# Optimization experiments

Hardware: AMD Instinct MI355X
Metric: run time of the kernel (lower is better)

The kernel has to match this reference:

```python
import jax, jax.numpy as jnp
import numpy as np

EMBED_DIM = 512
NUM_HEADS = 8
GLOBAL_MIX = 0.5


def setup_inputs() -> dict:
    key = jax.random.key(0)
    ks = jax.random.split(key, 7)
    B, L, E = 8, 1024, EMBED_DIM
    s = 1.0 / np.sqrt(E)
    x = jax.random.normal(ks[0], (B, L, E), dtype=jnp.float32)
    mask = jax.random.randint(ks[1], (B, L), 0, 2) > 0  # True = valid token
    Wq = jax.random.normal(ks[2], (E, E), dtype=jnp.float32) * s
    Wk = jax.random.normal(ks[3], (E, E), dtype=jnp.float32) * s
    Wv = jax.random.normal(ks[4], (E, E), dtype=jnp.float32) * s
    Wo = jax.random.normal(ks[5], (E, E), dtype=jnp.float32) * s
    G = jax.random.normal(ks[6], (L, L), dtype=jnp.float32)
    return {"x": x, "mask": mask, "Wq": Wq, "Wk": Wk, "Wv": Wv, "Wo": Wo, "G": G}


def _tanh_mha(x, mask, Wq, Wk, Wv, Wo, G):
    B, L, E = x.shape
    H = NUM_HEADS
    D = E // H
    scale = 1.0 / np.sqrt(D)
    dt = x.dtype
    fmax = jnp.finfo(dt).max
    tiny = jnp.finfo(dt).tiny

    def split_heads(t):  # (B,L,E) -> (B,H,L,D)
        return t.reshape(B, L, H, D).transpose(0, 2, 1, 3)

    q = split_heads(x @ Wq.T)
    k = split_heads(x @ Wk.T)
    v = split_heads(x @ Wv.T)

    scores = jnp.tanh(jnp.einsum('bhqd,bhkd->bhqk', q, k) * scale)
    key_valid = mask[:, None, None, :]  # (B,1,1,L)
    scores = jnp.where(key_valid, scores, -jnp.inf)

    finite = jnp.isfinite(scores)
    finite_scores = jnp.where(finite, scores, -fmax)
    m = jnp.max(finite_scores, axis=(1, 2, 3), keepdims=True)  # per-sample amax over heads+q+k
    m = jnp.where(jnp.isfinite(m), m, jnp.zeros_like(m))
    exp_scores = jnp.where(finite, jnp.exp(scores - m), jnp.zeros_like(scores))

    mf = mask.astype(dt)
    exp_scores = exp_scores * mf[:, None, None, :] * mf[:, None, :, None]
    denom = jnp.maximum(exp_scores.sum(axis=(1, 2, 3), keepdims=True), tiny)
    weights = exp_scores / denom
    # dropout p=0 -> identity; renorm pass kept for faithfulness
    renorm = jnp.maximum(weights.sum(axis=(1, 2, 3), keepdims=True), tiny)
    weights = weights / renorm

    # learnable global attention: softmax rows, clamp, mask, normalize over (q,k)
    activated = jnp.maximum(jax.nn.softmax(G, axis=-1), 0.0)  # (L,L)
    gscores = activated[None] * mf[:, None, :] * mf[:, :, None]  # (B,L,L)
    gsums = jnp.maximum(gscores.sum(axis=(1, 2), keepdims=True), tiny)
    gnorm = (gscores / gsums)[:, None]  # (B,1,L,L)
    weights = (1.0 - GLOBAL_MIX) * weights + GLOBAL_MIX * gnorm

    attended = jnp.einsum('bhqk,bhkd->bhqd', weights, v)
    attended = attended * mf[:, None, :, None]
    attended = attended.transpose(0, 2, 1, 3).reshape(B, L, E)
    return attended @ Wo.T


def reference(x, mask, Wq, Wk, Wv, Wo, G):
    return _tanh_mha(x, mask, Wq, Wk, Wv, Wo, G)
```

## Files before the change

kernel.cpp:

```cpp
#include <hip/hip_runtime.h>
#include <math.h>

#define B_ 8
#define L_ 1024
#define E_ 512
#define H_ 8
#define D_ 64
#define QSZ (B_*H_*L_*D_)
#define TINYF 1.175494350822287508e-38f

typedef unsigned short u16;
typedef __attribute__((ext_vector_type(8))) short bfrag;
typedef __attribute__((ext_vector_type(4))) float ffrag;
typedef __attribute__((ext_vector_type(16))) float ffrag16;
typedef __attribute__((ext_vector_type(4))) short vshort4;

#if __has_builtin(__builtin_amdgcn_exp2f)
#define EXP2F(x) __builtin_amdgcn_exp2f(x)
#else
#define EXP2F(x) __expf((x) * 0.6931471805599453f)
#endif
#if __has_builtin(__builtin_amdgcn_rcpf)
#define RCPF(x) __builtin_amdgcn_rcpf(x)
#else
#define RCPF(x) (1.0f / (x))
#endif

__device__ __forceinline__ u16 f2b(float f) {
  unsigned u = __float_as_uint(f);
  u += 0x7fffu + ((u >> 16) & 1u);
  return (u16)(u >> 16);
}
__device__ __forceinline__ unsigned pk2(float a, float b) {
  unsigned ua = __float_as_uint(a); ua += 0x7fffu + ((ua >> 16) & 1u);
  unsigned ub = __float_as_uint(b); ub += 0x7fffu + ((ub >> 16) & 1u);
  return (ua >> 16) | (ub & 0xffff0000u);
}
__device__ __forceinline__ float b2f(unsigned h) { return __uint_as_float(h << 16); }
__device__ __forceinline__ float blo(unsigned u) { return __uint_as_float(u << 16); }
__device__ __forceinline__ float bhi(unsigned u) { return __uint_as_float(u & 0xffff0000u); }

__device__ __forceinline__ bfrag cvt8v(const float* __restrict__ src) {
  float4 a = *(const float4*)src;
  float4 b = *(const float4*)(src + 4);
  bfrag r;
  r[0]=(short)f2b(a.x); r[1]=(short)f2b(a.y); r[2]=(short)f2b(a.z); r[3]=(short)f2b(a.w);
  r[4]=(short)f2b(b.x); r[5]=(short)f2b(b.y); r[6]=(short)f2b(b.z); r[7]=(short)f2b(b.w);
  return r;
}

__device__ __forceinline__ void gll16(const void* g, void* l) {
  __builtin_amdgcn_global_load_lds(
      (const __attribute__((address_space(1))) void*)g,
      (__attribute__((address_space(3))) void*)l, 16, 0, 0);
}

__global__ __launch_bounds__(256) void prep_k(
    const float* __restrict__ x, const float* __restrict__ Wq,
    const float* __restrict__ Wk, const float* __restrict__ Wv,
    const float* __restrict__ Wo, u16* __restrict__ xb, u16* __restrict__ Wb,
    float* __restrict__ sums) {
  const int bid = blockIdx.x, t = threadIdx.x;
  if (bid == 0 && t < 16) sums[t] = 0.0f;
  if (bid < 2048) {
    size_t c = (size_t)bid * 256 + t;
    *(bfrag*)&xb[c * 8] = cvt8v(x + c * 8);
  } else {
    const int c2 = bid - 2048;
    const float* src = (c2 < 128) ? Wq : (c2 < 256) ? Wk : (c2 < 384) ? Wv : Wo;
    const size_t base = (size_t)(c2 >> 7) * 262144;
    const size_t cc = (size_t)(c2 & 127) * 256 + t;
    *(bfrag*)&Wb[base + cc * 8] = cvt8v(src + cc * 8);
  }
}

__global__ __launch_bounds__(256) void softmax_g_k(
    const float* __restrict__ G, const int* __restrict__ mask,
    u16* __restrict__ actb, float* __restrict__ R) {
  const int q = blockIdx.x, t = threadIdx.x;
  const int w = t >> 6, lane = t & 63;
  __shared__ float sred[8];
  __shared__ float rred[4][8];
  float4 g4 = ((const float4*)(G + (size_t)q * 1024))[t];
  float m = fmaxf(fmaxf(g4.x, g4.y), fmaxf(g4.z, g4.w));
#pragma unroll
  for (int off = 32; off > 0; off >>= 1) m = fmaxf(m, __shfl_down(m, off));
  if (lane == 0) sred[w] = m;
  __syncthreads();
  m = fmaxf(fmaxf(sred[0], sred[1]), fmaxf(sred[2], sred[3]));
  float e0 = __expf(g4.x - m), e1 = __expf(g4.y - m);
  float e2 = __expf(g4.z - m), e3 = __expf(g4.w - m);
  float s = e0 + e1 + e2 + e3;
#pragma unroll
  for (int off = 32; off > 0; off >>= 1) s += __shfl_down(s, off);
  if (lane == 0) sred[4 + w] = s;
  __syncthreads();
  const float inv = 1.0f / (sred[4] + sred[5] + sred[6] + sred[7]);
  const unsigned p0 = pk2(e0 * inv, e1 * inv);
  const unsigned p1 = pk2(e2 * inv, e3 * inv);
  *(uint2*)&actb[(size_t)q * 1024 + t * 4] = make_uint2(p0, p1);
  const float r0 = blo(p0), r1 = bhi(p0);
  const float r2 = blo(p1), r3 = bhi(p1);
  float rd[8];
#pragma unroll
  for (int b = 0; b < 8; ++b) {
    const int* mkp = mask + b * 1024 + t * 4;
    rd[b] = (mkp[0] ? r0 : 0.f) + (mkp[1] ? r1 : 0.f) +
            (mkp[2] ? r2 : 0.f) + (mkp[3] ? r3 : 0.f);
#pragma unroll
    for (int off = 32; off > 0; off >>= 1) rd[b] += __shfl_down(rd[b], off);
  }
  if (lane == 0)
#pragma unroll
    for (int b = 0; b < 8; ++b) rred[w][b] = rd[b];
  __syncthreads();
  if (t < 8) R[q * 8 + t] = rred[0][t] + rred[1][t] + rred[2][t] + rred[3][t];
}

__global__ __launch_bounds__(256) void gsum_reduce_k(
    const float* __restrict__ R, const int* __restrict__ mask,
    float* __restrict__ sums) {
  const int t = threadIdx.x, w = t >> 6, lane = t & 63;
  __shared__ float rr[4][8];
  float acc[8] = {0,0,0,0,0,0,0,0};
  for (int q = t; q < 1024; q += 256)
#pragma unroll
    for (int b = 0; b < 8; ++b)
      if (mask[b * 1024 + q]) acc[b] += R[q * 8 + b];
#pragma unroll
  for (int b = 0; b < 8; ++b) {
#pragma unroll
    for (int off = 32; off > 0; off >>= 1) acc[b] += __shfl_down(acc[b], off);
  }
  if (lane == 0)
#pragma unroll
    for (int b = 0; b < 8; ++b) rr[w][b] = acc[b];
  __syncthreads();
  if (t < 8) sums[8 + t] = rr[0][t] + rr[1][t] + rr[2][t] + rr[3][t];
}

__global__ __launch_bounds__(256) void proj_k(
    const u16* __restrict__ xb, const u16* __restrict__ Wb,
    const int* __restrict__ mask,
    u16* __restrict__ Qb, u16* __restrict__ Kb, u16* __restrict__ Vtb) {
  const int m0 = blockIdx.x * 128;
  const int n0 = blockIdx.y * 64;
  __shared__ u16 As[128 * 64];
  __shared__ u16 Bs[64 * 64];
  const int t = threadIdx.x, w = t >> 6, lane = t & 63;
  const int l15 = lane & 15, quad = lane >> 4;
  const int x7 = l15 & 7;
  const ffrag fz = {0.f, 0.f, 0.f, 0.f};
  ffrag acc[2][4];
#pragma unroll
  for (int am = 0; am < 2; ++am)
#pragma unroll
    for (int bn = 0; bn < 4; ++bn) acc[am][bn] = fz;

  for (int kk = 0; kk < 512; kk += 64) {
    __syncthreads();
#pragma unroll
    for (int j = 0; j < 4; ++j) {
      const int c = w * 256 + j * 64 + lane;
      const int row = c >> 3, ck = (c & 7) ^ (row & 7);
      gll16(xb + (size_t)(m0 + row) * 512 + kk + ck * 8,
            &As[(size_t)(w * 256 + j * 64) * 8]);
    }
#pragma unroll
    for (int j = 0; j < 2; ++j) {
      const int c = w * 128 + j * 64 + lane;
      const int row = c >> 3, ck = (c & 7) ^ (row & 7);
      gll16(Wb + (size_t)(n0 + row) * 512 + kk + ck * 8,
            &Bs[(size_t)(w * 128 + j * 64) * 8]);
    }
    __syncthreads();
#pragma unroll
    for (int s = 0; s < 2; ++s) {
      const int co = ((quad + 4 * s) ^ x7) << 3;
      bfrag a0 = *(const bfrag*)&As[(w * 32 + l15) * 64 + co];
      bfrag a1 = *(const bfrag*)&As[(w * 32 + 16 + l15) * 64 + co];
#pragma unroll
      for (int bn = 0; bn < 4; ++bn) {
        bfrag bb = *(const bfrag*)&Bs[(bn * 16 + l15) * 64 + co];
        acc[0][bn] = __builtin_amdgcn_mfma_f32_16x16x32_bf16(a0, bb, acc[0][bn], 0, 0, 0);
        acc[1][bn] = __builtin_amdgcn_mfma_f32_16x16x32_bf16(a1, bb, acc[1][bn], 0, 0, 0);
      }
    }
  }
  const int z = n0 >> 9;
  const int c0 = n0 & 511;
#pragma unroll
  for (int am = 0; am < 2; ++am) {
    const int mbase = m0 + w * 32 + am * 16 + quad * 4;
    const int b = mbase >> 10, l0 = mbase & 1023;
#pragma unroll
    for (int bn = 0; bn < 4; ++bn) {
      const int nc = c0 + bn * 16 + l15;
      const int h = nc >> 6, d = nc & 63;
      if (z == 0) {
        u16* dst = Qb + ((size_t)(b * 8 + h) * 1024 + l0) * 64 + d;
#pragma unroll
        for (int r = 0; r < 4; ++r) dst[(size_t)r * 64] = f2b(acc[am][bn][r]);
      } else if (z == 1) {
        u16* dst = Kb + ((size_t)(b * 8 + h) * 1024 + l0) * 64 + d;
#pragma unroll
        for (int r = 0; r < 4; ++r) dst[(size_t)r * 64] = f2b(acc[am][bn][r]);
      } else {
        vshort4 vs;
#pragma unroll
        for (int r = 0; r < 4; ++r)
          vs[r] = (short)(mask[b * 1024 + l0 + r] ? f2b(acc[am][bn][r]) : (u16)0);
        *(vshort4*)(Vtb + ((size_t)(b * 8 + h) * 64 + d) * 1024 + l0) = vs;
      }
    }
  }
}

__global__ __launch_bounds__(256) void attn_k(
    const u16* __restrict__ Qb, const u16* __restrict__ Kb,
    const u16* __restrict__ Vtb, const u16* __restrict__ actb,
    const int* __restrict__ mask,
    u16* __restrict__ AEb, u16* __restrict__ AGb, float* __restrict__ denom) {
  const int qt = blockIdx.x;
  const int bh = blockIdx.y;
  const int b = bh >> 3, h = bh & 7;
  __shared__ __align__(16) u16 Ks[64 * 64];
  __shared__ __align__(16) u16 Vs[64 * 64];
  __shared__ __align__(16) u16 Acts[64 * 64];
  __shared__ __align__(16) u16 Es[64 * 64];
  __shared__ __align__(16) u16 Ms[16 * 64];
  const int t = threadIdx.x, w = t >> 6, lane = t & 63;
  const int l31 = lane & 31, hi = lane >> 5;
  const int qsb = w >> 1, msb = w & 1;
  const int qpb = w & 1, dpb = w >> 1;

  const u16* Kg = Kb + (size_t)bh * 65536;
  const u16* Vg = Vtb + (size_t)bh * 65536;
  const u16* Ag = actb + (size_t)(qt * 64) * 1024;

  const u16* Qrow = Qb + ((size_t)bh * 1024 + qt * 64 + qsb * 32 + l31) * 64;
  bfrag qf[4];
#pragma unroll
  for (int ko = 0; ko < 4; ++ko) qf[ko] = *(const bfrag*)(Qrow + ko * 16 + hi * 8);

  {
    int4 mi = *(const int4*)(mask + b * 1024 + t * 4);
    vshort4 mv;
    mv[0] = mi.x ? (short)0x3F80 : (short)0; mv[1] = mi.y ? (short)0x3F80 : (short)0;
    mv[2] = mi.z ? (short)0x3F80 : (short)0; mv[3] = mi.w ? (short)0x3F80 : (short)0;
    *(vshort4*)&Ms[t * 4] = mv;
  }

  auto stageK = [&](int kt) {
#pragma unroll
    for (int j = 0; j < 2; ++j) {
      const int c = w * 128 + j * 64 + lane;
      const int row = c >> 3, ck = (c & 7) ^ (row & 7);
      gll16(Kg + (size_t)(kt * 64 + row) * 64 + ck * 8,
            &Ks[(size_t)(w * 128 + j * 64) * 8]);
    }
  };
  auto stageV = [&](int kt) {
#pragma unroll
    for (int j = 0; j < 2; ++j) {
      const int c = w * 128 + j * 64 + lane;
      const int row = c >> 3, ck = (c & 7) ^ (row & 7);
      gll16(Vg + (size_t)row * 1024 + kt * 64 + ck * 8,
            &Vs[(size_t)(w * 128 + j * 64) * 8]);
    }
  };
  auto stageA = [&](int kt) {
#pragma unroll
    for (int j = 0; j < 2; ++j) {
      const int c = w * 128 + j * 64 + lane;
      const int row = c >> 3, ck = (c & 7) ^ (row & 7);
      gll16(Ag + (size_t)row * 1024 + kt * 64 + ck * 8,
            &Acts[(size_t)(w * 128 + j * 64) * 8]);
    }
  };

  stageK(0); stageV(0); stageA(0);
  __syncthreads();

  ffrag16 accE = {0.f}, accG = {0.f}, dacc = {0.f};
#pragma unroll
  for (int i = 0; i < 16; ++i) { accE[i] = 0.f; accG[i] = 0.f; dacc[i] = 0.f; }

  for (int kt = 0; kt < 16; ++kt) {
    ffrag16 st;
#pragma unroll
    for (int i = 0; i < 16; ++i) st[i] = 0.f;
    const int krow = msb * 32 + l31;
    const int kx7 = krow & 7;
#pragma unroll
    for (int ko = 0; ko < 4; ++ko) {
      bfrag ak = *(const bfrag*)&Ks[krow * 64 + (((ko * 2 + hi) ^ kx7) << 3)];
      st = __builtin_amdgcn_mfma_f32_32x32x16_bf16(ak, qf[ko], st, 0, 0, 0);
    }
    const int qrow = qsb * 32 + l31;
    const int qx7 = qrow & 7;
#pragma unroll
    for (int g = 0; g < 4; ++g) {
      float ee[4];
#pragma unroll
      for (int r = 0; r < 4; ++r) {
        const float tt = EXP2F(st[4 * g + r] * 0.360673760222f);
        ee[r] = EXP2F(RCPF(tt + 1.0f) * -2.88539008178f);
      }
      const int k0 = msb * 32 + g * 8 + hi * 4;
      *(uint2*)&Es[qrow * 64 + (((k0 >> 3) ^ qx7) << 3) + (k0 & 7)] =
          make_uint2(pk2(ee[0], ee[1]), pk2(ee[2], ee[3]));
    }
    __syncthreads();
    if (kt < 15) stageK(kt + 1);

    const int erow = qpb * 32 + l31;
    const int ex7 = erow & 7;
    const int vrow = dpb * 32 + l31;
    const int vx7 = vrow & 7;
#pragma unroll
    for (int ko = 0; ko < 4; ++ko) {
      const int ecs = ((ko * 2 + hi) ^ ex7) << 3;
      const int vcs = ((ko * 2 + hi) ^ vx7) << 3;
      bfrag ea = *(const bfrag*)&Es[erow * 64 + ecs];
      bfrag bv = *(const bfrag*)&Vs[vrow * 64 + vcs];
      accE = __builtin_amdgcn_mfma_f32_32x32x16_bf16(ea, bv, accE, 0, 0, 0);
      bfrag aa = *(const bfrag*)&Acts[erow * 64 + ecs];
      accG = __builtin_amdgcn_mfma_f32_32x32x16_bf16(aa, bv, accG, 0, 0, 0);
      if (w < 2) {
        bfrag bm = *(const bfrag*)&Ms[kt * 64 + ko * 16 + hi * 8];
        dacc = __builtin_amdgcn_mfma_f32_32x32x16_bf16(ea, bm, dacc, 0, 0, 0);
      }
    }
    __syncthreads();
    if (kt < 15) { stageV(kt + 1); stageA(kt + 1); }
  }

  const size_t obase = ((size_t)b * 1024 + qt * 64 + qpb * 32) * 512
                       + h * 64 + dpb * 32 + l31;
#pragma unroll
  for (int r = 0; r < 16; ++r) {
    const int qloc = (r & 3) + 8 * (r >> 2) + 4 * hi;
    AEb[obase + (size_t)qloc * 512] = f2b(accE[r]);
    AGb[obase + (size_t)qloc * 512] = f2b(accG[r]);
  }
  float dsumv = 0.0f;
  if (l31 == 0 && w < 2) {
    const int qb0 = b * 1024 + qt * 64 + qpb * 32 + 4 * hi;
#pragma unroll
    for (int r = 0; r < 16; ++r) {
      const int q = qb0 + (r & 3) + 8 * (r >> 2);
      dsumv += mask[q] ? dacc[r] : 0.0f;
    }
  }
  float* red4 = (float*)Es;
  if (l31 == 0 && w < 2) red4[w * 2 + hi] = dsumv;
  __syncthreads();
  if (t == 0) atomicAdd(denom + b, red4[0] + red4[1] + red4[2] + red4[3]);
}

__global__ __launch_bounds__(256) void o_proj_k(
    const u16* __restrict__ AEb, const u16* __restrict__ AGb,
    const int* __restrict__ mask, const float* __restrict__ sums,
    const u16* __restrict__ Wb, float* __restrict__ out) {
  const int m0 = blockIdx.x * 128;
  const int n0 = blockIdx.y * 64;
  const int b = m0 >> 10;
  const float c1 = 0.5f / fmaxf(sums[b], TINYF);
  const float c2 = 0.5f / fmaxf(sums[8 + b], TINYF);
  __shared__ __align__(16) u16 As[128 * 64];
  __shared__ __align__(16) u16 Bs[64 * 64];
  const int t = threadIdx.x, w = t >> 6, lane = t & 63;
  const int l15 = lane & 15, quad = lane >> 4;
  const int x7 = l15 & 7;
  int rowi[4]; float c1r[4], c2r[4];
#pragma unroll
  for (int i = 0; i < 4; ++i) {
    const int c = t + i * 256;
    rowi[i] = c >> 3;
    const int mq = mask[b * 1024 + ((m0 + rowi[i]) & 1023)];
    c1r[i] = mq ? c1 : 0.0f;
    c2r[i] = mq ? c2 : 0.0f;
  }
  const ffrag fz = {0.f, 0.f, 0.f, 0.f};
  ffrag acc[2][4];
#pragma unroll
  for (int am = 0; am < 2; ++am)
#pragma unroll
    for (int bn = 0; bn < 4; ++bn) acc[am][bn] = fz;

  for (int kk = 0; kk < 512; kk += 64) {
    __syncthreads();
#pragma unroll
    for (int i = 0; i < 4; ++i) {
      const int c = t + i * 256;
      const int row = rowi[i], ck = c & 7;
      const size_t gofs = (size_t)(m0 + row) * 512 + kk + ck * 8;
      uint4 ua = *(const uint4*)(AEb + gofs);
      uint4 ug = *(const uint4*)(AGb + gofs);
      const float a1 = c1r[i], a2 = c2r[i];
      uint4 res;
      res.x = pk2(a1 * blo(ua.x) + a2 * blo(ug.x), a1 * bhi(ua.x) + a2 * bhi(ug.x));
      res.y = pk2(a1 * blo(ua.y) + a2 * blo(ug.y), a1 * bhi(ua.y) + a2 * bhi(ug.y));
      res.z = pk2(a1 * blo(ua.z) + a2 * blo(ug.z), a1 * bhi(ua.z) + a2 * bhi(ug.z));
      res.w = pk2(a1 * blo(ua.w) + a2 * blo(ug.w), a1 * bhi(ua.w) + a2 * bhi(ug.w));
      *(uint4*)&As[row * 64 + ((ck ^ (row & 7)) << 3)] = res;
    }
#pragma unroll
    for (int j = 0; j < 2; ++j) {
      const int c = w * 128 + j * 64 + lane;
      const int row = c >> 3, ck = (c & 7) ^ (row & 7);
      gll16(Wb + (size_t)(1536 + n0 + row) * 512 + kk + ck * 8,
            &Bs[(size_t)(w * 128 + j * 64) * 8]);
    }
    __syncthreads();
#pragma unroll
    for (int s = 0; s < 2; ++s) {
      const int co = ((quad + 4 * s) ^ x7) << 3;
      bfrag a0 = *(const bfrag*)&As[(w * 32 + l15) * 64 + co];
      bfrag a1 = *(const bfrag*)&As[(w * 32 + 16 + l15) * 64 + co];
#pragma unroll
      for (int bn = 0; bn < 4; ++bn) {
        bfrag bb = *(const bfrag*)&Bs[(bn * 16 + l15) * 64 + co];
        acc[0][bn] = __builtin_amdgcn_mfma_f32_16x16x32_bf16(a0, bb, acc[0][bn], 0, 0, 0);
        acc[1][bn] = __builtin_amdgcn_mfma_f32_16x16x32_bf16(a1, bb, acc[1][bn], 0, 0, 0);
      }
    }
  }
#pragma unroll
  for (int am = 0; am < 2; ++am) {
    const int mbase = m0 + w * 32 + am * 16 + quad * 4;
#pragma unroll
    for (int bn = 0; bn < 4; ++bn) {
      const int n = n0 + bn * 16 + l15;
#pragma unroll
      for (int r = 0; r < 4; ++r)
        out[(size_t)(mbase + r) * 512 + n] = acc[am][bn][r];
    }
  }
}

extern "C" void kernel_launch(void* const* d_in, const int* in_sizes, int n_in,
                              void* d_out, int out_size, void* d_ws, size_t ws_size,
                              hipStream_t stream) {
  const float* x  = (const float*)d_in[0];
  const int* mask = (const int*)d_in[1];
  const float* Wq = (const float*)d_in[2];
  const float* Wk = (const float*)d_in[3];
  const float* Wv = (const float*)d_in[4];
  const float* Wo = (const float*)d_in[5];
  const float* G  = (const float*)d_in[6];
  float* out = (float*)d_out;

  u16* xb   = (u16*)d_ws;
  u16* Wb   = xb + (size_t)8192 * 512;
  u16* Qb   = Wb + (size_t)2048 * 512;
  u16* Kb   = Qb + QSZ;
  u16* Vtb  = Kb + QSZ;
  u16* actb = Vtb + QSZ;
  u16* AEb  = actb + (size_t)1024 * 1024;
  u16* AGb  = AEb + (size_t)B_ * L_ * E_;
  float* R  = (float*)(AGb + (size_t)B_ * L_ * E_);
  float* SUMS = R + 8192;

  prep_k<<<2560, 256, 0, stream>>>(x, Wq, Wk, Wv, Wo, xb, Wb, SUMS);
  softmax_g_k<<<1024, 256, 0, stream>>>(G, mask, actb, R);
  gsum_reduce_k<<<1, 256, 0, stream>>>(R, mask, SUMS);
  proj_k<<<dim3(64, 24), 256, 0, stream>>>(xb, Wb, mask, Qb, Kb, Vtb);
  attn_k<<<dim3(16, 64), 256, 0, stream>>>(Qb, Kb, Vtb, actb, mask, AEb, AGb, SUMS);
  o_proj_k<<<dim3(64, 8), 256, 0, stream>>>(AEb, AGb, mask, SUMS, Wb, out);
}
```

Baseline: 196.8 us.

## Enlarge attention query tile to 128 and fold G-sum reduction into atomics

The attention kernel now processes 128 queries per block, with each wave owning 32 query rows across all 64 keys and both D halves. Each staged K/V tile is therefore reused by twice as many queries, and the grid shrinks to half as many blocks. Each wave keeps its own E tile in shared memory, which removes the cross-wave dependency on Es and gives every wave a denominator MFMA. Separately, the single-block gsum_reduce kernel is removed: softmax_g_k atomically adds its masked row sums directly, saving one launch at the cost of more atomics and higher register and LDS use per block.

```diff
diff --git a/kernel.cpp b/kernel.cpp
--- a/kernel.cpp
+++ b/kernel.cpp
@@ -36,7 +36,6 @@
   unsigned ub = __float_as_uint(b); ub += 0x7fffu + ((ub >> 16) & 1u);
   return (ua >> 16) | (ub & 0xffff0000u);
 }
-__device__ __forceinline__ float b2f(unsigned h) { return __uint_as_float(h << 16); }
 __device__ __forceinline__ float blo(unsigned u) { return __uint_as_float(u << 16); }
 __device__ __forceinline__ float bhi(unsigned u) { return __uint_as_float(u & 0xffff0000u); }
 
@@ -76,7 +75,7 @@
 
 __global__ __launch_bounds__(256) void softmax_g_k(
     const float* __restrict__ G, const int* __restrict__ mask,
-    u16* __restrict__ actb, float* __restrict__ R) {
+    u16* __restrict__ actb, float* __restrict__ sums) {
   const int q = blockIdx.x, t = threadIdx.x;
   const int w = t >> 6, lane = t & 63;
   __shared__ float sred[8];
@@ -114,29 +113,10 @@
 #pragma unroll
     for (int b = 0; b < 8; ++b) rred[w][b] = rd[b];
   __syncthreads();
-  if (t < 8) R[q * 8 + t] = rred[0][t] + rred[1][t] + rred[2][t] + rred[3][t];
-}
-
-__global__ __launch_bounds__(256) void gsum_reduce_k(
-    const float* __restrict__ R, const int* __restrict__ mask,
-    float* __restrict__ sums) {
-  const int t = threadIdx.x, w = t >> 6, lane = t & 63;
-  __shared__ float rr[4][8];
-  float acc[8] = {0,0,0,0,0,0,0,0};
-  for (int q = t; q < 1024; q += 256)
-#pragma unroll
-    for (int b = 0; b < 8; ++b)
-      if (mask[b * 1024 + q]) acc[b] += R[q * 8 + b];
-#pragma unroll
-  for (int b = 0; b < 8; ++b) {
-#pragma unroll
-    for (int off = 32; off > 0; off >>= 1) acc[b] += __shfl_down(acc[b], off);
-  }
-  if (lane == 0)
-#pragma unroll
-    for (int b = 0; b < 8; ++b) rr[w][b] = acc[b];
-  __syncthreads();
-  if (t < 8) sums[8 + t] = rr[0][t] + rr[1][t] + rr[2][t] + rr[3][t];
+  if (t < 8) {
+    if (mask[t * 1024 + q])
+      atomicAdd(sums + 8 + t, rred[0][t] + rred[1][t] + rred[2][t] + rred[3][t]);
+  }
 }
 
 __global__ __launch_bounds__(256) void proj_k(
@@ -226,19 +206,18 @@
   const int b = bh >> 3, h = bh & 7;
   __shared__ __align__(16) u16 Ks[64 * 64];
   __shared__ __align__(16) u16 Vs[64 * 64];
-  __shared__ __align__(16) u16 Acts[64 * 64];
-  __shared__ __align__(16) u16 Es[64 * 64];
+  __shared__ __align__(16) u16 Acts[128 * 64];
+  __shared__ __align__(16) u16 Es[4][32 * 64];
   __shared__ __align__(16) u16 Ms[16 * 64];
   const int t = threadIdx.x, w = t >> 6, lane = t & 63;
   const int l31 = lane & 31, hi = lane >> 5;
-  const int qsb = w >> 1, msb = w & 1;
-  const int qpb = w & 1, dpb = w >> 1;
+  const int r7 = l31 & 7;
 
   const u16* Kg = Kb + (size_t)bh * 65536;
   const u16* Vg = Vtb + (size_t)bh * 65536;
-  const u16* Ag = actb + (size_t)(qt * 64) * 1024;
-
-  const u16* Qrow = Qb + ((size_t)bh * 1024 + qt * 64 + qsb * 32 + l31) * 64;
+  const u16* Ag = actb + (size_t)(qt * 128) * 1024;
+
+  const u16* Qrow = Qb + ((size_t)bh * 1024 + qt * 128 + w * 32 + l31) * 64;
   bfrag qf[4];
 #pragma unroll
   for (int ko = 0; ko < 4; ++ko) qf[ko] = *(const bfrag*)(Qrow + ko * 16 + hi * 8);
@@ -271,92 +250,105 @@
   };
   auto stageA = [&](int kt) {
 #pragma unroll
-    for (int j = 0; j < 2; ++j) {
-      const int c = w * 128 + j * 64 + lane;
+    for (int j = 0; j < 4; ++j) {
+      const int c = w * 256 + j * 64 + lane;
       const int row = c >> 3, ck = (c & 7) ^ (row & 7);
       gll16(Ag + (size_t)row * 1024 + kt * 64 + ck * 8,
-            &Acts[(size_t)(w * 128 + j * 64) * 8]);
+            &Acts[(size_t)(w * 256 + j * 64) * 8]);
     }
   };
 
   stageK(0); stageV(0); stageA(0);
   __syncthreads();
 
-  ffrag16 accE = {0.f}, accG = {0.f}, dacc = {0.f};
-#pragma unroll
-  for (int i = 0; i < 16; ++i) { accE[i] = 0.f; accG[i] = 0.f; dacc[i] = 0.f; }
+  ffrag16 accE[2], accG[2], dacc;
+#pragma unroll
+  for (int i = 0; i < 16; ++i) { accE[0][i]=0.f; accE[1][i]=0.f; accG[0][i]=0.f; accG[1][i]=0.f; dacc[i]=0.f; }
+
+  u16* Ew = Es[w];
 
   for (int kt = 0; kt < 16; ++kt) {
-    ffrag16 st;
-#pragma unroll
-    for (int i = 0; i < 16; ++i) st[i] = 0.f;
-    const int krow = msb * 32 + l31;
-    const int kx7 = krow & 7;
+    ffrag16 st[2];
+#pragma unroll
+    for (int i = 0; i < 16; ++i) { st[0][i] = 0.f; st[1][i] = 0.f; }
+#pragma unroll
+    for (int mb = 0; mb < 2; ++mb) {
+      const int krow = mb * 32 + l31;
+      const int kx7 = krow & 7;
+#pragma unroll
+      for (int ko = 0; ko < 4; ++ko) {
+        bfrag ak = *(const bfrag*)&Ks[krow * 64 + (((ko * 2 + hi) ^ kx7) << 3)];
+        st[mb] = __builtin_amdgcn_mfma_f32_32x32x16_bf16(ak, qf[ko], st[mb], 0, 0, 0);
+      }
+    }
+#pragma unroll
+    for (int mb = 0; mb < 2; ++mb) {
+#pragma unroll
+      for (int g = 0; g < 4; ++g) {
+        float ee[4];
+#pragma unroll
+        for (int r = 0; r < 4; ++r) {
+          const float tt = EXP2F(st[mb][4 * g + r] * 0.360673760222f);
+          ee[r] = EXP2F(RCPF(tt + 1.0f) * -2.88539008178f);
+        }
+        const int k0 = mb * 32 + g * 8 + hi * 4;
+        *(uint2*)&Ew[l31 * 64 + (((k0 >> 3) ^ r7) << 3) + (k0 & 7)] =
+            make_uint2(pk2(ee[0], ee[1]), pk2(ee[2], ee[3]));
+      }
+    }
+    __syncthreads();
+    if (kt < 15) stageK(kt + 1);
+
+    const int arow = w * 32 + l31;
 #pragma unroll
     for (int ko = 0; ko < 4; ++ko) {
-      bfrag ak = *(const bfrag*)&Ks[krow * 64 + (((ko * 2 + hi) ^ kx7) << 3)];
-      st = __builtin_amdgcn_mfma_f32_32x32x16_bf16(ak, qf[ko], st, 0, 0, 0);
-    }
-    const int qrow = qsb * 32 + l31;
-    const int qx7 = qrow & 7;
-#pragma unroll
-    for (int g = 0; g < 4; ++g) {
-      float ee[4];
-#pragma unroll
-      for (int r = 0; r < 4; ++r) {
-        const float tt = EXP2F(st[4 * g + r] * 0.360673760222f);
-        ee[r] = EXP2F(RCPF(tt + 1.0f) * -2.88539008178f);
-      }
-      const int k0 = msb * 32 + g * 8 + hi * 4;
-      *(uint2*)&Es[qrow * 64 + (((k0 >> 3) ^ qx7) << 3) + (k0 & 7)] =
-          make_uint2(pk2(ee[0], ee[1]), pk2(ee[2], ee[3]));
-    }
-    __syncthreads();
-    if (kt < 15) stageK(kt + 1);
-
-    const int erow = qpb * 32 + l31;
-    const int ex7 = erow & 7;
-    const int vrow = dpb * 32 + l31;
-    const int vx7 = vrow & 7;
-#pragma unroll
-    for (int ko = 0; ko < 4; ++ko) {
-      const int ecs = ((ko * 2 + hi) ^ ex7) << 3;
-      const int vcs = ((ko * 2 + hi) ^ vx7) << 3;
-      bfrag ea = *(const bfrag*)&Es[erow * 64 + ecs];
-      bfrag bv = *(const bfrag*)&Vs[vrow * 64 + vcs];
-      accE = __builtin_amdgcn_mfma_f32_32x32x16_bf16(ea, bv, accE, 0, 0, 0);
-      bfrag aa = *(const bfrag*)&Acts[erow * 64 + ecs];
-      accG = __builtin_amdgcn_mfma_f32_32x32x16_bf16(aa, bv, accG, 0, 0, 0);
-      if (w < 2) {
-        bfrag bm = *(const bfrag*)&Ms[kt * 64 + ko * 16 + hi * 8];
-        dacc = __builtin_amdgcn_mfma_f32_32x32x16_bf16(ea, bm, dacc, 0, 0, 0);
+      const int cs = ((ko * 2 + hi) ^ r7) << 3;
+      bfrag ea = *(const bfrag*)&Ew[l31 * 64 + cs];
+      bfrag aa = *(const bfrag*)&Acts[arow * 64 + cs];
+      bfrag bm = *(const bfrag*)&Ms[kt * 64 + ko * 16 + hi * 8];
+      dacc = __builtin_amdgcn_mfma_f32_32x32x16_bf16(ea, bm, dacc, 0, 0, 0);
+#pragma unroll
+      for (int db = 0; db < 2; ++db) {
+        const int vrow = db * 32 + l31;
+        bfrag bv = *(const bfrag*)&Vs[vrow * 64 + (((ko * 2 + hi) ^ (vrow & 7)) << 3)];
+        accE[db] = __builtin_amdgcn_mfma_f32_32x32x16_bf16(ea, bv, accE[db], 0, 0, 0);
+        accG[db] = __builtin_amdgcn_mfma_f32_32x32x16_bf16(aa, bv, accG[db], 0, 0, 0);
       }
     }
     __syncthreads();
     if (kt < 15) { stageV(kt + 1); stageA(kt + 1); }
   }
 
-  const size_t obase = ((size_t)b * 1024 + qt * 64 + qpb * 32) * 512
-                       + h * 64 + dpb * 32 + l31;
-#pragma unroll
-  for (int r = 0; r < 16; ++r) {
-    const int qloc = (r & 3) + 8 * (r >> 2) + 4 * hi;
-    AEb[obase + (size_t)qloc * 512] = f2b(accE[r]);
-    AGb[obase + (size_t)qloc * 512] = f2b(accG[r]);
-  }
+#pragma unroll
+  for (int db = 0; db < 2; ++db) {
+    const size_t obase = ((size_t)(b * 1024 + qt * 128 + w * 32)) * 512
+                         + h * 64 + db * 32 + l31;
+#pragma unroll
+    for (int r = 0; r < 16; ++r) {
+      const int qloc = (r & 3) + 8 * (r >> 2) + 4 * hi;
+      AEb[obase + (size_t)qloc * 512] = f2b(accE[db][r]);
+      AGb[obase + (size_t)qloc * 512] = f2b(accG[db][r]);
+    }
+  }
+  __syncthreads();
   float dsumv = 0.0f;
-  if (l31 == 0 && w < 2) {
-    const int qb0 = b * 1024 + qt * 64 + qpb * 32 + 4 * hi;
+  if (l31 == 0) {
+    const int qb0 = b * 1024 + qt * 128 + w * 32 + 4 * hi;
 #pragma unroll
     for (int r = 0; r < 16; ++r) {
       const int q = qb0 + (r & 3) + 8 * (r >> 2);
       dsumv += mask[q] ? dacc[r] : 0.0f;
     }
   }
-  float* red4 = (float*)Es;
-  if (l31 == 0 && w < 2) red4[w * 2 + hi] = dsumv;
-  __syncthreads();
-  if (t == 0) atomicAdd(denom + b, red4[0] + red4[1] + red4[2] + red4[3]);
+  float* red = (float*)Ms;
+  if (l31 == 0) red[w * 2 + hi] = dsumv;
+  __syncthreads();
+  if (t == 0) {
+    float tot = 0.f;
+#pragma unroll
+    for (int i = 0; i < 8; ++i) tot += red[i];
+    atomicAdd(denom + b, tot);
+  }
 }
 
 __global__ __launch_bounds__(256) void o_proj_k(
@@ -460,13 +452,11 @@
   u16* actb = Vtb + QSZ;
   u16* AEb  = actb + (size_t)1024 * 1024;
   u16* AGb  = AEb + (size_t)B_ * L_ * E_;
-  float* R  = (float*)(AGb + (size_t)B_ * L_ * E_);
-  float* SUMS = R + 8192;
+  float* SUMS = (float*)(AGb + (size_t)B_ * L_ * E_);
 
   prep_k<<<2560, 256, 0, stream>>>(x, Wq, Wk, Wv, Wo, xb, Wb, SUMS);
-  softmax_g_k<<<1024, 256, 0, stream>>>(G, mask, actb, R);
-  gsum_reduce_k<<<1, 256, 0, stream>>>(R, mask, SUMS);
+  softmax_g_k<<<1024, 256, 0, stream>>>(G, mask, actb, SUMS);
   proj_k<<<dim3(64, 24), 256, 0, stream>>>(xb, Wb, mask, Qb, Kb, Vtb);
-  attn_k<<<dim3(16, 64), 256, 0, stream>>>(Qb, Kb, Vtb, actb, mask, AEb, AGb, SUMS);
+  attn_k<<<dim3(8, 64), 256, 0, stream>>>(Qb, Kb, Vtb, actb, mask, AEb, AGb, SUMS);
   o_proj_k<<<dim3(64, 8), 256, 0, stream>>>(AEb, AGb, mask, SUMS, Wb, out);
 }
```

Result: slower. 211.2 us (+7.3%).

## Split attention over key halves and fold small prep kernels into neighbors

Applied to the files above, without the earlier changes.

Attention now runs a third grid dimension that splits the 1024 keys into two halves. Each half writes its own partial AE/AG buffers, and the output projection sums the two partials while loading. The G-softmax kernel is merged into the bf16 conversion kernel, and the global-sum reduction plus zeroing of sums moves into one block of the projection kernel, removing two launches. The LDS swizzle now also mixes in row>>3, and the ad-hoc reuse of shared memory as a reduction buffer becomes a dedicated array. In exchange there is double the intermediate traffic, extra reads in o_proj, and warps w and w+2 appear to compute the same PV outputs redundantly.

```diff
diff --git a/kernel.cpp b/kernel.cpp
--- a/kernel.cpp
+++ b/kernel.cpp
@@ -7,7 +7,9 @@
 #define H_ 8
 #define D_ 64
 #define QSZ (B_*H_*L_*D_)
+#define BLE ((size_t)B_*L_*E_)
 #define TINYF 1.175494350822287508e-38f
+#define SWK(r) ((((r) ^ ((r) >> 3))) & 7)
 
 typedef unsigned short u16;
 typedef __attribute__((ext_vector_type(8))) short bfrag;
@@ -36,7 +38,6 @@
   unsigned ub = __float_as_uint(b); ub += 0x7fffu + ((ub >> 16) & 1u);
   return (ua >> 16) | (ub & 0xffff0000u);
 }
-__device__ __forceinline__ float b2f(unsigned h) { return __uint_as_float(h << 16); }
 __device__ __forceinline__ float blo(unsigned u) { return __uint_as_float(u << 16); }
 __device__ __forceinline__ float bhi(unsigned u) { return __uint_as_float(u & 0xffff0000u); }
 
@@ -55,32 +56,31 @@
       (__attribute__((address_space(3))) void*)l, 16, 0, 0);
 }
 
-__global__ __launch_bounds__(256) void prep_k(
+__global__ __launch_bounds__(256) void prep_softmax_k(
     const float* __restrict__ x, const float* __restrict__ Wq,
     const float* __restrict__ Wk, const float* __restrict__ Wv,
-    const float* __restrict__ Wo, u16* __restrict__ xb, u16* __restrict__ Wb,
-    float* __restrict__ sums) {
+    const float* __restrict__ Wo, const float* __restrict__ G,
+    const int* __restrict__ mask,
+    u16* __restrict__ xb, u16* __restrict__ Wb, u16* __restrict__ actb,
+    float* __restrict__ R) {
   const int bid = blockIdx.x, t = threadIdx.x;
-  if (bid == 0 && t < 16) sums[t] = 0.0f;
+  __shared__ float sred[8];
+  __shared__ float rred[4][8];
   if (bid < 2048) {
     size_t c = (size_t)bid * 256 + t;
     *(bfrag*)&xb[c * 8] = cvt8v(x + c * 8);
-  } else {
+    return;
+  }
+  if (bid < 2560) {
     const int c2 = bid - 2048;
     const float* src = (c2 < 128) ? Wq : (c2 < 256) ? Wk : (c2 < 384) ? Wv : Wo;
     const size_t base = (size_t)(c2 >> 7) * 262144;
     const size_t cc = (size_t)(c2 & 127) * 256 + t;
     *(bfrag*)&Wb[base + cc * 8] = cvt8v(src + cc * 8);
-  }
-}
-
-__global__ __launch_bounds__(256) void softmax_g_k(
-    const float* __restrict__ G, const int* __restrict__ mask,
-    u16* __restrict__ actb, float* __restrict__ R) {
-  const int q = blockIdx.x, t = threadIdx.x;
+    return;
+  }
+  const int q = bid - 2560;
   const int w = t >> 6, lane = t & 63;
-  __shared__ float sred[8];
-  __shared__ float rred[4][8];
   float4 g4 = ((const float4*)(G + (size_t)q * 1024))[t];
   float m = fmaxf(fmaxf(g4.x, g4.y), fmaxf(g4.z, g4.w));
 #pragma unroll
@@ -117,39 +117,41 @@
   if (t < 8) R[q * 8 + t] = rred[0][t] + rred[1][t] + rred[2][t] + rred[3][t];
 }
 
-__global__ __launch_bounds__(256) void gsum_reduce_k(
-    const float* __restrict__ R, const int* __restrict__ mask,
-    float* __restrict__ sums) {
-  const int t = threadIdx.x, w = t >> 6, lane = t & 63;
-  __shared__ float rr[4][8];
-  float acc[8] = {0,0,0,0,0,0,0,0};
-  for (int q = t; q < 1024; q += 256)
-#pragma unroll
-    for (int b = 0; b < 8; ++b)
-      if (mask[b * 1024 + q]) acc[b] += R[q * 8 + b];
-#pragma unroll
-  for (int b = 0; b < 8; ++b) {
-#pragma unroll
-    for (int off = 32; off > 0; off >>= 1) acc[b] += __shfl_down(acc[b], off);
-  }
-  if (lane == 0)
-#pragma unroll
-    for (int b = 0; b < 8; ++b) rr[w][b] = acc[b];
-  __syncthreads();
-  if (t < 8) sums[8 + t] = rr[0][t] + rr[1][t] + rr[2][t] + rr[3][t];
-}
-
 __global__ __launch_bounds__(256) void proj_k(
     const u16* __restrict__ xb, const u16* __restrict__ Wb,
-    const int* __restrict__ mask,
+    const int* __restrict__ mask, const float* __restrict__ R,
+    float* __restrict__ sums,
     u16* __restrict__ Qb, u16* __restrict__ Kb, u16* __restrict__ Vtb) {
   const int m0 = blockIdx.x * 128;
   const int n0 = blockIdx.y * 64;
   __shared__ u16 As[128 * 64];
   __shared__ u16 Bs[64 * 64];
+  __shared__ float rr[4][8];
   const int t = threadIdx.x, w = t >> 6, lane = t & 63;
   const int l15 = lane & 15, quad = lane >> 4;
   const int x7 = l15 & 7;
+
+  if (blockIdx.x == 0 && blockIdx.y == 0) {
+    float a8[8] = {0,0,0,0,0,0,0,0};
+    for (int q = t; q < 1024; q += 256)
+#pragma unroll
+      for (int b = 0; b < 8; ++b)
+        if (mask[b * 1024 + q]) a8[b] += R[q * 8 + b];
+#pragma unroll
+    for (int b = 0; b < 8; ++b) {
+#pragma unroll
+      for (int off = 32; off > 0; off >>= 1) a8[b] += __shfl_down(a8[b], off);
+    }
+    if (lane == 0)
+#pragma unroll
+      for (int b = 0; b < 8; ++b) rr[w][b] = a8[b];
+    __syncthreads();
+    if (t < 8) {
+      sums[t] = 0.0f;
+      sums[8 + t] = rr[0][t] + rr[1][t] + rr[2][t] + rr[3][t];
+    }
+  }
+
   const ffrag fz = {0.f, 0.f, 0.f, 0.f};
   ffrag acc[2][4];
 #pragma unroll
@@ -223,28 +225,32 @@
     u16* __restrict__ AEb, u16* __restrict__ AGb, float* __restrict__ denom) {
   const int qt = blockIdx.x;
   const int bh = blockIdx.y;
+  const int ks = blockIdx.z;
   const int b = bh >> 3, h = bh & 7;
   __shared__ __align__(16) u16 Ks[64 * 64];
   __shared__ __align__(16) u16 Vs[64 * 64];
   __shared__ __align__(16) u16 Acts[64 * 64];
   __shared__ __align__(16) u16 Es[64 * 64];
-  __shared__ __align__(16) u16 Ms[16 * 64];
+  __shared__ __align__(16) u16 Ms[512];
+  __shared__ float red4[4];
   const int t = threadIdx.x, w = t >> 6, lane = t & 63;
   const int l31 = lane & 31, hi = lane >> 5;
   const int qsb = w >> 1, msb = w & 1;
-  const int qpb = w & 1, dpb = w >> 1;
-
-  const u16* Kg = Kb + (size_t)bh * 65536;
-  const u16* Vg = Vtb + (size_t)bh * 65536;
-  const u16* Ag = actb + (size_t)(qt * 64) * 1024;
+  const int qpb = w & 1;
+
+  const u16* Kg = Kb + (size_t)bh * 65536 + (size_t)ks * 512 * 64;
+  const u16* Vg = Vtb + (size_t)bh * 65536 + ks * 512;
+  const u16* Ag = actb + (size_t)(qt * 64) * 1024 + ks * 512;
+  u16* AEp = AEb + (size_t)ks * BLE;
+  u16* AGp = AGb + (size_t)ks * BLE;
 
   const u16* Qrow = Qb + ((size_t)bh * 1024 + qt * 64 + qsb * 32 + l31) * 64;
   bfrag qf[4];
 #pragma unroll
   for (int ko = 0; ko < 4; ++ko) qf[ko] = *(const bfrag*)(Qrow + ko * 16 + hi * 8);
 
-  {
-    int4 mi = *(const int4*)(mask + b * 1024 + t * 4);
+  if (t < 128) {
+    int4 mi = *(const int4*)(mask + b * 1024 + ks * 512 + t * 4);
     vshort4 mv;
     mv[0] = mi.x ? (short)0x3F80 : (short)0; mv[1] = mi.y ? (short)0x3F80 : (short)0;
     mv[2] = mi.z ? (short)0x3F80 : (short)0; mv[3] = mi.w ? (short)0x3F80 : (short)0;
@@ -255,7 +261,7 @@
 #pragma unroll
     for (int j = 0; j < 2; ++j) {
       const int c = w * 128 + j * 64 + lane;
-      const int row = c >> 3, ck = (c & 7) ^ (row & 7);
+      const int row = c >> 3, ck = (c & 7) ^ SWK(row);
       gll16(Kg + (size_t)(kt * 64 + row) * 64 + ck * 8,
             &Ks[(size_t)(w * 128 + j * 64) * 8]);
     }
@@ -264,7 +270,7 @@
 #pragma unroll
     for (int j = 0; j < 2; ++j) {
       const int c = w * 128 + j * 64 + lane;
-      const int row = c >> 3, ck = (c & 7) ^ (row & 7);
+      const int row = c >> 3, ck = (c & 7) ^ SWK(row);
       gll16(Vg + (size_t)row * 1024 + kt * 64 + ck * 8,
             &Vs[(size_t)(w * 128 + j * 64) * 8]);
     }
@@ -273,7 +279,7 @@
 #pragma unroll
     for (int j = 0; j < 2; ++j) {
       const int c = w * 128 + j * 64 + lane;
-      const int row = c >> 3, ck = (c & 7) ^ (row & 7);
+      const int row = c >> 3, ck = (c & 7) ^ SWK(row);
       gll16(Ag + (size_t)row * 1024 + kt * 64 + ck * 8,
             &Acts[(size_t)(w * 128 + j * 64) * 8]);
     }
@@ -282,23 +288,26 @@
   stageK(0); stageV(0); stageA(0);
   __syncthreads();
 
-  ffrag16 accE = {0.f}, accG = {0.f}, dacc = {0.f};
-#pragma unroll
-  for (int i = 0; i < 16; ++i) { accE[i] = 0.f; accG[i] = 0.f; dacc[i] = 0.f; }
-
-  for (int kt = 0; kt < 16; ++kt) {
+  ffrag16 accE[2], accG[2], dacc;
+#pragma unroll
+  for (int i = 0; i < 16; ++i) {
+    accE[0][i] = 0.f; accE[1][i] = 0.f; accG[0][i] = 0.f; accG[1][i] = 0.f;
+    dacc[i] = 0.f;
+  }
+
+  for (int kt = 0; kt < 8; ++kt) {
     ffrag16 st;
 #pragma unroll
     for (int i = 0; i < 16; ++i) st[i] = 0.f;
     const int krow = msb * 32 + l31;
-    const int kx7 = krow & 7;
+    const int kk7 = SWK(krow);
 #pragma unroll
     for (int ko = 0; ko < 4; ++ko) {
-      bfrag ak = *(const bfrag*)&Ks[krow * 64 + (((ko * 2 + hi) ^ kx7) << 3)];
+      bfrag ak = *(const bfrag*)&Ks[krow * 64 + (((ko * 2 + hi) ^ kk7) << 3)];
       st = __builtin_amdgcn_mfma_f32_32x32x16_bf16(ak, qf[ko], st, 0, 0, 0);
     }
     const int qrow = qsb * 32 + l31;
-    const int qx7 = qrow & 7;
+    const int qk7 = SWK(qrow);
 #pragma unroll
     for (int g = 0; g < 4; ++g) {
       float ee[4];
@@ -308,41 +317,45 @@
         ee[r] = EXP2F(RCPF(tt + 1.0f) * -2.88539008178f);
       }
       const int k0 = msb * 32 + g * 8 + hi * 4;
-      *(uint2*)&Es[qrow * 64 + (((k0 >> 3) ^ qx7) << 3) + (k0 & 7)] =
+      *(uint2*)&Es[qrow * 64 + (((k0 >> 3) ^ qk7) << 3) + (k0 & 7)] =
           make_uint2(pk2(ee[0], ee[1]), pk2(ee[2], ee[3]));
     }
     __syncthreads();
-    if (kt < 15) stageK(kt + 1);
+    if (kt < 7) stageK(kt + 1);
 
     const int erow = qpb * 32 + l31;
-    const int ex7 = erow & 7;
-    const int vrow = dpb * 32 + l31;
-    const int vx7 = vrow & 7;
+    const int ek7 = SWK(erow);
 #pragma unroll
     for (int ko = 0; ko < 4; ++ko) {
-      const int ecs = ((ko * 2 + hi) ^ ex7) << 3;
-      const int vcs = ((ko * 2 + hi) ^ vx7) << 3;
-      bfrag ea = *(const bfrag*)&Es[erow * 64 + ecs];
-      bfrag bv = *(const bfrag*)&Vs[vrow * 64 + vcs];
-      accE = __builtin_amdgcn_mfma_f32_32x32x16_bf16(ea, bv, accE, 0, 0, 0);
-      bfrag aa = *(const bfrag*)&Acts[erow * 64 + ecs];
-      accG = __builtin_amdgcn_mfma_f32_32x32x16_bf16(aa, bv, accG, 0, 0, 0);
+      const int co = ko * 2 + hi;
+      bfrag ea = *(const bfrag*)&Es[erow * 64 + ((co ^ ek7) << 3)];
+      bfrag aa = *(const bfrag*)&Acts[erow * 64 + ((co ^ ek7) << 3)];
       if (w < 2) {
         bfrag bm = *(const bfrag*)&Ms[kt * 64 + ko * 16 + hi * 8];
         dacc = __builtin_amdgcn_mfma_f32_32x32x16_bf16(ea, bm, dacc, 0, 0, 0);
       }
-    }
-    __syncthreads();
-    if (kt < 15) { stageV(kt + 1); stageA(kt + 1); }
-  }
-
-  const size_t obase = ((size_t)b * 1024 + qt * 64 + qpb * 32) * 512
-                       + h * 64 + dpb * 32 + l31;
-#pragma unroll
-  for (int r = 0; r < 16; ++r) {
-    const int qloc = (r & 3) + 8 * (r >> 2) + 4 * hi;
-    AEb[obase + (size_t)qloc * 512] = f2b(accE[r]);
-    AGb[obase + (size_t)qloc * 512] = f2b(accG[r]);
+#pragma unroll
+      for (int db = 0; db < 2; ++db) {
+        const int vrow = db * 32 + l31;
+        bfrag bv = *(const bfrag*)&Vs[vrow * 64 + ((co ^ SWK(vrow)) << 3)];
+        accE[db] = __builtin_amdgcn_mfma_f32_32x32x16_bf16(ea, bv, accE[db], 0, 0, 0);
+        accG[db] = __builtin_amdgcn_mfma_f32_32x32x16_bf16(aa, bv, accG[db], 0, 0, 0);
+      }
+    }
+    __syncthreads();
+    if (kt < 7) { stageV(kt + 1); stageA(kt + 1); }
+  }
+
+#pragma unroll
+  for (int db = 0; db < 2; ++db) {
+    const size_t obase = ((size_t)(b * 1024 + qt * 64 + qpb * 32)) * 512
+                         + h * 64 + db * 32 + l31;
+#pragma unroll
+    for (int r = 0; r < 16; ++r) {
+      const int qloc = (r & 3) + 8 * (r >> 2) + 4 * hi;
+      AEp[obase + (size_t)qloc * 512] = f2b(accE[db][r]);
+      AGp[obase + (size_t)qloc * 512] = f2b(accG[db][r]);
+    }
   }
   float dsumv = 0.0f;
   if (l31 == 0 && w < 2) {
@@ -352,9 +365,8 @@
       const int q = qb0 + (r & 3) + 8 * (r >> 2);
       dsumv += mask[q] ? dacc[r] : 0.0f;
     }
-  }
-  float* red4 = (float*)Es;
-  if (l31 == 0 && w < 2) red4[w * 2 + hi] = dsumv;
+    red4[w * 2 + hi] = dsumv;
+  }
   __syncthreads();
   if (t == 0) atomicAdd(denom + b, red4[0] + red4[1] + red4[2] + red4[3]);
 }
@@ -396,14 +408,20 @@
       const int c = t + i * 256;
       const int row = rowi[i], ck = c & 7;
       const size_t gofs = (size_t)(m0 + row) * 512 + kk + ck * 8;
-      uint4 ua = *(const uint4*)(AEb + gofs);
-      uint4 ug = *(const uint4*)(AGb + gofs);
+      uint4 ua0 = *(const uint4*)(AEb + gofs);
+      uint4 ua1 = *(const uint4*)(AEb + BLE + gofs);
+      uint4 ug0 = *(const uint4*)(AGb + gofs);
+      uint4 ug1 = *(const uint4*)(AGb + BLE + gofs);
       const float a1 = c1r[i], a2 = c2r[i];
       uint4 res;
-      res.x = pk2(a1 * blo(ua.x) + a2 * blo(ug.x), a1 * bhi(ua.x) + a2 * bhi(ug.x));
-      res.y = pk2(a1 * blo(ua.y) + a2 * blo(ug.y), a1 * bhi(ua.y) + a2 * bhi(ug.y));
-      res.z = pk2(a1 * blo(ua.z) + a2 * blo(ug.z), a1 * bhi(ua.z) + a2 * bhi(ug.z));
-      res.w = pk2(a1 * blo(ua.w) + a2 * blo(ug.w), a1 * bhi(ua.w) + a2 * bhi(ug.w));
+      res.x = pk2(a1 * (blo(ua0.x) + blo(ua1.x)) + a2 * (blo(ug0.x) + blo(ug1.x)),
+                  a1 * (bhi(ua0.x) + bhi(ua1.x)) + a2 * (bhi(ug0.x) + bhi(ug1.x)));
+      res.y = pk2(a1 * (blo(ua0.y) + blo(ua1.y)) + a2 * (blo(ug0.y) + blo(ug1.y)),
+                  a1 * (bhi(ua0.y) + bhi(ua1.y)) + a2 * (bhi(ug0.y) + bhi(ug1.y)));
+      res.z = pk2(a1 * (blo(ua0.z) + blo(ua1.z)) + a2 * (blo(ug0.z) + blo(ug1.z)),
+                  a1 * (bhi(ua0.z) + bhi(ua1.z)) + a2 * (bhi(ug0.z) + bhi(ug1.z)));
+      res.w = pk2(a1 * (blo(ua0.w) + blo(ua1.w)) + a2 * (blo(ug0.w) + blo(ug1.w)),
+                  a1 * (bhi(ua0.w) + bhi(ua1.w)) + a2 * (bhi(ug0.w) + bhi(ug1.w)));
       *(uint4*)&As[row * 64 + ((ck ^ (row & 7)) << 3)] = res;
     }
 #pragma unroll
@@ -459,14 +477,12 @@
   u16* Vtb  = Kb + QSZ;
   u16* actb = Vtb + QSZ;
   u16* AEb  = actb + (size_t)1024 * 1024;
-  u16* AGb  = AEb + (size_t)B_ * L_ * E_;
-  float* R  = (float*)(AGb + (size_t)B_ * L_ * E_);
+  u16* AGb  = AEb + 2 * BLE;
+  float* R  = (float*)(AGb + 2 * BLE);
   float* SUMS = R + 8192;
 
-  prep_k<<<2560, 256, 0, stream>>>(x, Wq, Wk, Wv, Wo, xb, Wb, SUMS);
-  softmax_g_k<<<1024, 256, 0, stream>>>(G, mask, actb, R);
-  gsum_reduce_k<<<1, 256, 0, stream>>>(R, mask, SUMS);
-  proj_k<<<dim3(64, 24), 256, 0, stream>>>(xb, Wb, mask, Qb, Kb, Vtb);
-  attn_k<<<dim3(16, 64), 256, 0, stream>>>(Qb, Kb, Vtb, actb, mask, AEb, AGb, SUMS);
+  prep_softmax_k<<<3584, 256, 0, stream>>>(x, Wq, Wk, Wv, Wo, G, mask, xb, Wb, actb, R);
+  proj_k<<<dim3(64, 24), 256, 0, stream>>>(xb, Wb, mask, R, SUMS, Qb, Kb, Vtb);
+  attn_k<<<dim3(16, 64, 2), 256, 0, stream>>>(Qb, Kb, Vtb, actb, mask, AEb, AGb, SUMS);
   o_proj_k<<<dim3(64, 8), 256, 0, stream>>>(AEb, AGb, mask, SUMS, Wb, out);
 }
```

After: 225.0 us. 1.14x slower.
